# Optimization experiments

Hardware: AMD Instinct MI355X
Metric: run time of the kernel (lower is better)

The kernel has to match this reference:

```python
import jax, jax.numpy as jnp
import numpy as np

B, N, M, ZD, YD, XD = 4, 512, 512, 128, 2, 1


def setup_inputs() -> dict:
    key = jax.random.key(0)
    k_t, k_z, k_x, k_w = jax.random.split(key, 4)
    return {
        "t": jax.random.normal(k_t, (B, N, XD), dtype=jnp.float32),
        "z": jax.random.normal(k_z, (B, N, ZD), dtype=jnp.float32),
        "x": jax.random.normal(k_x, (B, M, XD), dtype=jnp.float32),
        "sigma": jnp.zeros((ZD,), dtype=jnp.float32),  # log(length_scale=1) = 0
        "W": jax.random.normal(k_w, (YD, ZD), dtype=jnp.float32) * (1.0 / np.sqrt(ZD)),
        "b": jnp.zeros((YD,), dtype=jnp.float32),
    }


def reference(t, z, x, sigma, W, b):
    # diff: (b, n, m) -- sum over x_dim as in the torch code, then channelized
    diff = (x[:, None, :, :] - t[:, :, None, :]).sum(-1)
    scale = jnp.exp(sigma)  # (c,)
    # kernel: (b, n, m, c) RBF weights per channel
    kernel = jnp.exp(-0.5 * (diff[..., None] / scale) ** 2)
    # z-weighted reduction over grid points n -> (b, m, c)
    y = jnp.einsum("bnc,bnmc->bmc", z, kernel)
    # final linear: (b, m, y_dim)
    return y @ W.T + b
```

## Files before the change

kernel.cpp:

```cpp
#include <hip/hip_runtime.h>
#include <math.h>

#define B_  4
#define N_  512
#define M_  512
#define ZD_ 128
#define YD_ 2
#define XD_ 1

#define GROUPS 2
#define TM     2
#define BLOCK  (GROUPS * ZD_)
#define NSPLIT 4
#define NCHUNK (N_ / NSPLIT)

#define LOG2E_HALF 0.72134752044f

__global__ __launch_bounds__(BLOCK)
void decoder_kernel(const float* __restrict__ t,
                    const float* __restrict__ z,
                    const float* __restrict__ x,
                    const float* __restrict__ sigma,
                    const float* __restrict__ W,
                    const float* __restrict__ bias,
                    float* __restrict__ out)
{
    __shared__ float2 ts2[NCHUNK];
    __shared__ float  accs[GROUPS * TM * ZD_];

    const int b   = blockIdx.y;
    const int nz  = blockIdx.z;
    const int n0  = nz * NCHUNK;
    const int tid = threadIdx.x;
    const int mi  = tid >> 7;
    const int c   = tid & (ZD_ - 1);
    const int m0  = (blockIdx.x * GROUPS + mi) * TM;

    if (tid < NCHUNK) {
        const float tv = t[(size_t)b * N_ + n0 + tid];
        ts2[tid] = make_float2(tv, tv * tv);
    }
    __syncthreads();

    const float sc = __expf(sigma[c]);
    const float a2 = -LOG2E_HALF / (sc * sc);

    float Bx[TM], E[TM];
    #pragma unroll
    for (int j = 0; j < TM; ++j) {
        const float xv = x[(size_t)b * M_ + m0 + j];
        Bx[j] = -2.0f * a2 * xv;
        E[j]  = __builtin_amdgcn_exp2f(a2 * xv * xv);
    }

    const float* zp = z + ((size_t)b * N_ + n0) * ZD_ + c;

    float acc[TM];
    #pragma unroll
    for (int j = 0; j < TM; ++j) acc[j] = 0.f;

    #pragma unroll 8
    for (int n = 0; n < NCHUNK; ++n) {
        const float  zv = zp[(size_t)n * ZD_];
        const float2 tt = ts2[n];
        const float  w  = a2 * tt.y;
        #pragma unroll
        for (int j = 0; j < TM; ++j) {
            const float p = fmaf(Bx[j], tt.x, w);
            const float e = __builtin_amdgcn_exp2f(p);
            acc[j] = fmaf(zv, e, acc[j]);
        }
    }

    #pragma unroll
    for (int j = 0; j < TM; ++j)
        accs[(mi * TM + j) * ZD_ + c] = E[j] * acc[j];
    __syncthreads();

    if (tid < GROUPS * TM * 32) {
        const int g = tid >> 5;
        const int l = tid & 31;
        float s0 = 0.f, s1 = 0.f;
        #pragma unroll
        for (int k = 0; k < 4; ++k) {
            const int cc = l + 32 * k;
            const float av = accs[g * ZD_ + cc];
            s0 = fmaf(W[cc], av, s0);
            s1 = fmaf(W[ZD_ + cc], av, s1);
        }
        #pragma unroll
        for (int d = 16; d >= 1; d >>= 1) {
            s0 += __shfl_xor(s0, d);
            s1 += __shfl_xor(s1, d);
        }
        if (l == 0) {
            const int m = (blockIdx.x * GROUPS + (g / TM)) * TM + (g % TM);
            const float b0 = (nz == 0) ? bias[0] : 0.f;
            const float b1 = (nz == 0) ? bias[1] : 0.f;
            atomicAdd(out + ((size_t)b * M_ + m) * YD_ + 0, s0 + b0);
            atomicAdd(out + ((size_t)b * M_ + m) * YD_ + 1, s1 + b1);
        }
    }
}

extern "C" void kernel_launch(void* const* d_in, const int* in_sizes, int n_in,
                              void* d_out, int out_size, void* d_ws, size_t ws_size,
                              hipStream_t stream) {
    const float* t     = (const float*)d_in[0];
    const float* z     = (const float*)d_in[1];
    const float* x     = (const float*)d_in[2];
    const float* sigma = (const float*)d_in[3];
    const float* W     = (const float*)d_in[4];
    const float* bias  = (const float*)d_in[5];
    float* out = (float*)d_out;

    hipMemsetAsync(out, 0, (size_t)out_size * sizeof(float), stream);

    dim3 grid(M_ / (GROUPS * TM), B_, NSPLIT);
    dim3 block(BLOCK);
    decoder_kernel<<<grid, block, 0, stream>>>(t, z, x, sigma, W, bias, out);
}
```

Before: 83.05 us.

## Raise per-thread m tile to 8 and split n across two sub-groups per block

Each thread now computes 8 output points instead of 2, so every z load is reused across more exp computations. The two 128-thread halves of a block now split the block's n-chunk instead of covering different m, and their partials are summed in shared memory before the W projection. NSPLIT doubles to 8 so the grid keeps enough blocks. The trade-off is more atomics per output and higher register pressure from the larger accumulator array.

```diff
diff --git a/kernel.cpp b/kernel.cpp
--- a/kernel.cpp
+++ b/kernel.cpp
@@ -8,11 +8,12 @@
 #define YD_ 2
 #define XD_ 1
 
-#define GROUPS 2
-#define TM     2
-#define BLOCK  (GROUPS * ZD_)
-#define NSPLIT 4
-#define NCHUNK (N_ / NSPLIT)
+#define TM      8
+#define NSUB    2
+#define BLOCK   (NSUB * ZD_)
+#define NSPLIT  8
+#define NBLOCKCHUNK (N_ / NSPLIT)
+#define NCHUNK  (NBLOCKCHUNK / NSUB)
 
 #define LOG2E_HALF 0.72134752044f
 
@@ -25,18 +26,18 @@
                     const float* __restrict__ bias,
                     float* __restrict__ out)
 {
-    __shared__ float2 ts2[NCHUNK];
-    __shared__ float  accs[GROUPS * TM * ZD_];
+    __shared__ float2 ts2[NBLOCKCHUNK];
+    __shared__ float  accs[NSUB][TM][ZD_];
 
     const int b   = blockIdx.y;
     const int nz  = blockIdx.z;
-    const int n0  = nz * NCHUNK;
+    const int n0  = nz * NBLOCKCHUNK;
     const int tid = threadIdx.x;
-    const int mi  = tid >> 7;
+    const int sg  = tid >> 7;
     const int c   = tid & (ZD_ - 1);
-    const int m0  = (blockIdx.x * GROUPS + mi) * TM;
+    const int m0  = blockIdx.x * TM;
 
-    if (tid < NCHUNK) {
+    if (tid < NBLOCKCHUNK) {
         const float tv = t[(size_t)b * N_ + n0 + tid];
         ts2[tid] = make_float2(tv, tv * tv);
     }
@@ -53,16 +54,16 @@
         E[j]  = __builtin_amdgcn_exp2f(a2 * xv * xv);
     }
 
-    const float* zp = z + ((size_t)b * N_ + n0) * ZD_ + c;
+    const float* zp = z + ((size_t)b * N_ + n0 + sg * NCHUNK) * ZD_ + c;
 
     float acc[TM];
     #pragma unroll
     for (int j = 0; j < TM; ++j) acc[j] = 0.f;
 
-    #pragma unroll 8
+    #pragma unroll 4
     for (int n = 0; n < NCHUNK; ++n) {
         const float  zv = zp[(size_t)n * ZD_];
-        const float2 tt = ts2[n];
+        const float2 tt = ts2[sg * NCHUNK + n];
         const float  w  = a2 * tt.y;
         #pragma unroll
         for (int j = 0; j < TM; ++j) {
@@ -74,17 +75,17 @@
 
     #pragma unroll
     for (int j = 0; j < TM; ++j)
-        accs[(mi * TM + j) * ZD_ + c] = E[j] * acc[j];
+        accs[sg][j][c] = E[j] * acc[j];
     __syncthreads();
 
-    if (tid < GROUPS * TM * 32) {
+    {
         const int g = tid >> 5;
         const int l = tid & 31;
         float s0 = 0.f, s1 = 0.f;
         #pragma unroll
         for (int k = 0; k < 4; ++k) {
             const int cc = l + 32 * k;
-            const float av = accs[g * ZD_ + cc];
+            const float av = accs[0][g][cc] + accs[1][g][cc];
             s0 = fmaf(W[cc], av, s0);
             s1 = fmaf(W[ZD_ + cc], av, s1);
         }
@@ -94,11 +95,10 @@
             s1 += __shfl_xor(s1, d);
         }
         if (l == 0) {
-            const int m = (blockIdx.x * GROUPS + (g / TM)) * TM + (g % TM);
             const float b0 = (nz == 0) ? bias[0] : 0.f;
             const float b1 = (nz == 0) ? bias[1] : 0.f;
-            atomicAdd(out + ((size_t)b * M_ + m) * YD_ + 0, s0 + b0);
-            atomicAdd(out + ((size_t)b * M_ + m) * YD_ + 1, s1 + b1);
+            atomicAdd(out + ((size_t)b * M_ + m0 + g) * YD_ + 0, s0 + b0);
+            atomicAdd(out + ((size_t)b * M_ + m0 + g) * YD_ + 1, s1 + b1);
         }
     }
 }
@@ -116,7 +116,7 @@
 
     hipMemsetAsync(out, 0, (size_t)out_size * sizeof(float), stream);
 
-    dim3 grid(M_ / (GROUPS * TM), B_, NSPLIT);
+    dim3 grid(M_ / TM, B_, NSPLIT);
     dim3 block(BLOCK);
     decoder_kernel<<<grid, block, 0, stream>>>(t, z, x, sigma, W, bias, out);
 }
```

After: 80.23 us. 3.4% less time.
